# Kernel tuning notes

Hardware: AMD Instinct MI355X
Metric: run time of the kernel (lower is better)

## Reference

```python
import jax, jax.numpy as jnp
import numpy as np

EPS = 1e-5
C = 128
B = 16384
SYMBIOTIC = 4.0
NUM_PARENTS = 16
CHILDREN_PER_PARENT = 7


def _inverse(v):
    # torch: sort -> rank -> reversed rank -> gather sorted values
    idx0 = np.argsort(v, kind='stable')
    value = v[idx0]
    idx1 = np.argsort(idx0, kind='stable')  # ranks
    idx2 = v.shape[0] - 1 - idx1
    return value[idx2]


def _build_stats():
    counts = np.floor(50000.0 * 0.97 ** np.arange(C)) + 1.0  # long-tailed
    N = counts.sum()
    weight = (N / counts).astype(np.float32)
    prior = np.eye(C, dtype=np.float32)
    for p in range(NUM_PARENTS):
        ch = NUM_PARENTS + CHILDREN_PER_PARENT * p + np.arange(CHILDREN_PER_PARENT)
        prior[p, ch] = 1.0
    prior_me = (prior == 0).astype(np.float32)          # 1 - prior, keep only exact 1s
    prior_ms = prior - np.eye(C, dtype=np.float32)      # prior (0/1) minus eye
    v1_sig = np.log(N / counts - 1.0 + EPS).astype(np.float32)
    v2_sig = _inverse(v1_sig).astype(np.float32)
    v1_sm = np.log(counts / N + EPS).astype(np.float32)
    v2_sm = _inverse(v1_sm).astype(np.float32)
    return weight, prior_me, prior_ms, v1_sig, v2_sig, v1_sm, v2_sm


def setup_inputs() -> dict:
    key = jax.random.key(0)
    k1, k2 = jax.random.split(key)
    weight, prior_me, prior_ms, v1s, v2s, v1m, v2m = _build_stats()
    logits = 0.5 * jax.random.normal(k1, (12, B, C), dtype=jnp.float32)
    target = (jax.random.uniform(k2, (B, C)) < 0.1).astype(jnp.float32)
    return {
        'logits': logits, 'target': target,
        'weight': jnp.asarray(weight),
        'prior_me': jnp.asarray(prior_me), 'prior_ms': jnp.asarray(prior_ms),
        'v1_sigmoid': jnp.asarray(v1s), 'v2_sigmoid': jnp.asarray(v2s),
        'v1_softmax': jnp.asarray(v1m), 'v2_softmax': jnp.asarray(v2m),
    }


def reference(logits, target, weight, prior_me, prior_ms,
              v1_sigmoid, v2_sigmoid, v1_softmax, v2_softmax):
    zero = jnp.zeros_like(v1_sigmoid)
    # experts 0-5: sigmoid variants (long-tailed / balanced / inversed, twice)
    sig_shift = jnp.stack([zero, v1_sigmoid, v1_sigmoid - v2_sigmoid] * 2)  # [6,C]
    a_sig = jax.nn.sigmoid(logits[:6] - sig_shift[:, None, :])
    # experts 6-11: local-softmax variants
    sm_shift = jnp.stack([zero, v1_softmax, v1_softmax - v2_softmax] * 2)   # [6,C]
    e = jnp.exp(logits[6:] + sm_shift[:, None, :])                          # [6,B,C]
    denom = jnp.einsum('ebc,cd->ebd', e, prior_me) + e
    a_sm = e / (denom + EPS)
    acti = jnp.clip(jnp.concatenate([a_sig, a_sm], axis=0), EPS, 1.0 - EPS)  # [12,B,C]
    # weighted BCE per expert, summed
    bce = -weight * (target * jnp.log(acti) + (1.0 - target) * jnp.log(1.0 - acti))
    loss = jnp.sum(jnp.mean(bce, axis=(1, 2)))
    # symbiotic regularizer on experts 3,4,5,9,10,11
    row_sum = jnp.sum(prior_ms, axis=1)                 # [C]
    n_nz = jnp.sum(row_sum > 0).astype(acti.dtype)
    bsz = acti.shape[1]

    def symb(a):  # a: [B,C] activated logits
        def step(acc, xs):
            mask_row, parent = xs                       # [C], [B]
            term = jnp.log1p(jnp.exp(a - parent[:, None]))  # [B,C]
            rs = jnp.sum(mask_row)
            contrib = jnp.where(rs > 0, jnp.sum(term * mask_row) / (bsz * rs), 0.0)
            return acc + contrib, None
        total, _ = jax.lax.scan(step, jnp.float32(0.0), (prior_ms, a.T))
        return total / n_nz

    reg = jax.vmap(symb)(acti[jnp.array([3, 4, 5, 9, 10, 11])])
    return loss + SYMBIOTIC * jnp.sum(reg)
```

## Files before the change

### kernel.cpp

```cpp
#include <hip/hip_runtime.h>
#include <math.h>

#define CC 128
#define BB 16384
#define MEPS 1e-5f
#define LEPS  (-11.512925464970229f)
#define L1ME  (-1.0000050000287824e-05f)
#define NBLK 2048


__global__ __launch_bounds__(256) void mel_main(
    const float* __restrict__ logits, const float* __restrict__ target,
    const float* __restrict__ weight,
    const float* __restrict__ v1s, const float* __restrict__ v2s,
    const float* __restrict__ v1m, const float* __restrict__ v2m,
    float* __restrict__ partial)
{
    const int lane = threadIdx.x & 63;
    const int wib  = threadIdx.x >> 6;
    const int wave = blockIdx.x * 4 + wib;
    const int b0   = wave * 2;

    const int c0 = lane * 2;
    const int c1 = c0 + 1;

    const float w0 = weight[c0], w1 = weight[c1];
    const float s1a = v1s[c0], s1b = v1s[c1];
    const float s2a = v2s[c0], s2b = v2s[c1];
    const float m1a = v1m[c0], m1b = v1m[c1];
    const float m2a = v2m[c0], m2b = v2m[c1];

    const float sshift0[3] = {0.f, s1a, s1a - s2a};
    const float sshift1[3] = {0.f, s1b, s1b - s2b};
    const float mshift0[3] = {0.f, m1a, m1a - m2a};
    const float mshift1[3] = {0.f, m1b, m1b - m2b};

    const float childf = (lane >= 8) ? 1.f : 0.f;
    const int p0 = (c0 >= 16) ? (c0 - 16) / 7 : 0;
    const int p1 = (c1 >= 16) ? (c1 - 16) / 7 : 0;
    const int p0lane = p0 >> 1; const int p0sel = p0 & 1;
    const int p1lane = p1 >> 1; const int p1sel = p1 & 1;

    float2 tg[2], xs[6][2], xm[6][2];
    #pragma unroll
    for (int r = 0; r < 2; ++r) {
        const size_t ro = (size_t)(b0 + r) * CC + c0;
        tg[r] = *(const float2*)(target + ro);
        #pragma unroll
        for (int e = 0; e < 6; ++e)
            xs[e][r] = *(const float2*)(logits + (size_t)e * ((size_t)BB * CC) + ro);
        #pragma unroll
        for (int j = 0; j < 6; ++j)
            xm[j][r] = *(const float2*)(logits + (size_t)(6 + j) * ((size_t)BB * CC) + ro);
    }

    float acc_bce  = 0.f;
    float acc_symb = 0.f;

    #pragma unroll
    for (int r = 0; r < 2; ++r) {
        const bool t0 = tg[r].x > 0.5f;
        const bool t1 = tg[r].y > 0.5f;

        #pragma unroll
        for (int e = 0; e < 6; ++e) {
            const int si = e % 3;
            const float z0 = xs[e][r].x - sshift0[si];
            const float z1 = xs[e][r].y - sshift1[si];
            const float ex0 = __expf(-z0), ex1 = __expf(-z1);
            const float sp0 = __logf(1.f + ex0), sp1 = __logf(1.f + ex1);
            const float la0  = fminf(fmaxf(-sp0,      LEPS), L1ME);
            const float l1a0 = fminf(fmaxf(-z0 - sp0, LEPS), L1ME);
            const float la1  = fminf(fmaxf(-sp1,      LEPS), L1ME);
            const float l1a1 = fminf(fmaxf(-z1 - sp1, LEPS), L1ME);
            acc_bce += w0 * (t0 ? la0 : l1a0);
            acc_bce += w1 * (t1 ? la1 : l1a1);
            if (e >= 3) {
                const float a0 = __builtin_amdgcn_rcpf(1.f + ex0);
                const float a1 = __builtin_amdgcn_rcpf(1.f + ex1);
                const float ca0 = fminf(fmaxf(a0, MEPS), 1.f - MEPS);
                const float ca1 = fminf(fmaxf(a1, MEPS), 1.f - MEPS);
                const float qa0 = __shfl(ca0, p0lane, 64);
                const float qb0 = __shfl(ca1, p0lane, 64);
                const float cap0 = p0sel ? qb0 : qa0;
                const float qa1 = __shfl(ca0, p1lane, 64);
                const float qb1 = __shfl(ca1, p1lane, 64);
                const float cap1 = p1sel ? qb1 : qa1;
                acc_symb += childf * __logf(1.f + __expf(ca0 - cap0));
                acc_symb += childf * __logf(1.f + __expf(ca1 - cap1));
            }
        }

        #pragma unroll
        for (int j = 0; j < 6; ++j) {
            const int si = j % 3;
            const float e0 = __expf(xm[j][r].x + mshift0[si]);
            const float e1 = __expf(xm[j][r].y + mshift1[si]);
            float S = e0 + e1;
            #pragma unroll
            for (int off = 32; off > 0; off >>= 1)
                S += __shfl_xor(S, off, 64);
            const float qa0 = __shfl(e0, p0lane, 64);
            const float qb0 = __shfl(e1, p0lane, 64);
            const float ep0 = p0sel ? qb0 : qa0;
            const float qa1 = __shfl(e0, p1lane, 64);
            const float qb1 = __shfl(e1, p1lane, 64);
            const float ep1 = p1sel ? qb1 : qa1;

            const float den0 = S + MEPS - childf * ep0;
            const float den1 = S + MEPS - childf * ep1;
            float a0 = e0 * __builtin_amdgcn_rcpf(den0);
            float a1 = e1 * __builtin_amdgcn_rcpf(den1);
            a0 = fminf(fmaxf(a0, MEPS), 1.f - MEPS);
            a1 = fminf(fmaxf(a1, MEPS), 1.f - MEPS);
            const float arg0 = t0 ? a0 : 1.f - a0;
            const float arg1 = t1 ? a1 : 1.f - a1;
            acc_bce += w0 * __logf(arg0);
            acc_bce += w1 * __logf(arg1);
            if (j >= 3) {
                const float rS = __builtin_amdgcn_rcpf(S + MEPS);
                float ap0 = ep0 * rS, ap1 = ep1 * rS;
                ap0 = fminf(fmaxf(ap0, MEPS), 1.f - MEPS);
                ap1 = fminf(fmaxf(ap1, MEPS), 1.f - MEPS);
                acc_symb += childf * __logf(1.f + __expf(a0 - ap0));
                acc_symb += childf * __logf(1.f + __expf(a1 - ap1));
            }
        }
    }

    float val = -acc_bce * (1.f / ((float)BB * (float)CC))
              + acc_symb * (4.f / (112.f * (float)BB));

    #pragma unroll
    for (int off = 32; off > 0; off >>= 1)
        val += __shfl_xor(val, off, 64);

    __shared__ float sdata[4];
    if (lane == 0) sdata[wib] = val;
    __syncthreads();
    if (threadIdx.x == 0)
        partial[blockIdx.x] = sdata[0] + sdata[1] + sdata[2] + sdata[3];
}

__global__ __launch_bounds__(256) void mel_reduce(
    const float* __restrict__ partial, float* __restrict__ out)
{
    float v = 0.f;
    #pragma unroll
    for (int i = 0; i < NBLK / 256; ++i)
        v += partial[threadIdx.x + i * 256];
    #pragma unroll
    for (int off = 32; off > 0; off >>= 1)
        v += __shfl_xor(v, off, 64);
    __shared__ float s[4];
    const int lane = threadIdx.x & 63, wib = threadIdx.x >> 6;
    if (lane == 0) s[wib] = v;
    __syncthreads();
    if (threadIdx.x == 0) out[0] = s[0] + s[1] + s[2] + s[3];
}

extern "C" void kernel_launch(void* const* d_in, const int* in_sizes, int n_in,
                              void* d_out, int out_size, void* d_ws, size_t ws_size,
                              hipStream_t stream) {
    const float* logits = (const float*)d_in[0];
    const float* target = (const float*)d_in[1];
    const float* weight = (const float*)d_in[2];
    const float* v1s = (const float*)d_in[5];
    const float* v2s = (const float*)d_in[6];
    const float* v1m = (const float*)d_in[7];
    const float* v2m = (const float*)d_in[8];
    float* partial = (float*)d_ws;
    float* out = (float*)d_out;

    mel_main<<<NBLK, 256, 0, stream>>>(logits, target, weight,
                                       v1s, v2s, v1m, v2m, partial);
    mel_reduce<<<1, 256, 0, stream>>>(partial, out);
}
```

Baseline: 172.5 us.

## Remap lanes to four columns per row and use LDS for parent lookups

Each half-wave now handles one row, with each lane owning four consecutive columns. Loads become float4, and the six softmax row sums are reduced together over five interleaved shuffle steps instead of a full-wave reduction per expert. Parent activations are staged in per-wave shared memory and read back by index, replacing many cross-lane shuffles and selects. The sigmoid BCE clamp is dropped in favour of the plain softplus form, which cuts instructions in this compute-bound kernel but can differ slightly when logits fall outside the clamp range.

```diff
diff --git a/kernel.cpp b/kernel.cpp
--- a/kernel.cpp
+++ b/kernel.cpp
@@ -4,8 +4,6 @@
 #define CC 128
 #define BB 16384
 #define MEPS 1e-5f
-#define LEPS  (-11.512925464970229f)
-#define L1ME  (-1.0000050000287824e-05f)
 #define NBLK 2048
 
 
@@ -19,117 +17,126 @@
     const int lane = threadIdx.x & 63;
     const int wib  = threadIdx.x >> 6;
     const int wave = blockIdx.x * 4 + wib;
-    const int b0   = wave * 2;
+    const int r    = lane >> 5;
+    const int c    = lane & 31;
+    const int row  = wave * 2 + r;
 
-    const int c0 = lane * 2;
-    const int c1 = c0 + 1;
+    const float4 wtv = ((const float4*)weight)[c];
+    const float4 s1v = ((const float4*)v1s)[c];
+    const float4 s2v = ((const float4*)v2s)[c];
+    const float4 m1v = ((const float4*)v1m)[c];
+    const float4 m2v = ((const float4*)v2m)[c];
+    const float wt[4] = {wtv.x, wtv.y, wtv.z, wtv.w};
+    const float sv[3][4] = {{0.f,0.f,0.f,0.f},
+                            {s1v.x, s1v.y, s1v.z, s1v.w},
+                            {s1v.x-s2v.x, s1v.y-s2v.y, s1v.z-s2v.z, s1v.w-s2v.w}};
+    const float mv[3][4] = {{0.f,0.f,0.f,0.f},
+                            {m1v.x, m1v.y, m1v.z, m1v.w},
+                            {m1v.x-m2v.x, m1v.y-m2v.y, m1v.z-m2v.z, m1v.w-m2v.w}};
 
-    const float w0 = weight[c0], w1 = weight[c1];
-    const float s1a = v1s[c0], s1b = v1s[c1];
-    const float s2a = v2s[c0], s2b = v2s[c1];
-    const float m1a = v1m[c0], m1b = v1m[c1];
-    const float m2a = v2m[c0], m2b = v2m[c1];
+    const float childf = (c >= 4) ? 1.f : 0.f;
+    int pidx[4];
+    #pragma unroll
+    for (int k = 0; k < 4; ++k) {
+        const int ch = 4*c + k;
+        pidx[k] = (ch >= 16) ? (ch - 16) / 7 : 0;
+    }
 
-    const float sshift0[3] = {0.f, s1a, s1a - s2a};
-    const float sshift1[3] = {0.f, s1b, s1b - s2b};
-    const float mshift0[3] = {0.f, m1a, m1a - m2a};
-    const float mshift1[3] = {0.f, m1b, m1b - m2b};
+    float tg[4], xs[6][4], xm[6][4];
+    {
+        const size_t ro = (size_t)row * CC;
+        const float4 t4 = ((const float4*)(target + ro))[c];
+        tg[0]=t4.x; tg[1]=t4.y; tg[2]=t4.z; tg[3]=t4.w;
+        #pragma unroll
+        for (int e = 0; e < 6; ++e) {
+            const float4 v = ((const float4*)(logits + (size_t)e*(size_t)BB*CC + ro))[c];
+            xs[e][0]=v.x; xs[e][1]=v.y; xs[e][2]=v.z; xs[e][3]=v.w;
+        }
+        #pragma unroll
+        for (int j = 0; j < 6; ++j) {
+            const float4 v = ((const float4*)(logits + (size_t)(6+j)*(size_t)BB*CC + ro))[c];
+            xm[j][0]=v.x; xm[j][1]=v.y; xm[j][2]=v.z; xm[j][3]=v.w;
+        }
+    }
 
-    const float childf = (lane >= 8) ? 1.f : 0.f;
-    const int p0 = (c0 >= 16) ? (c0 - 16) / 7 : 0;
-    const int p1 = (c1 >= 16) ? (c1 - 16) / 7 : 0;
-    const int p0lane = p0 >> 1; const int p0sel = p0 & 1;
-    const int p1lane = p1 >> 1; const int p1sel = p1 & 1;
+    float accP = 0.f;
+    float accS = 0.f;
 
-    float2 tg[2], xs[6][2], xm[6][2];
+    float ca[3][4];
     #pragma unroll
-    for (int r = 0; r < 2; ++r) {
-        const size_t ro = (size_t)(b0 + r) * CC + c0;
-        tg[r] = *(const float2*)(target + ro);
+    for (int e = 0; e < 6; ++e) {
+        const int si = e % 3;
         #pragma unroll
-        for (int e = 0; e < 6; ++e)
-            xs[e][r] = *(const float2*)(logits + (size_t)e * ((size_t)BB * CC) + ro);
+        for (int k = 0; k < 4; ++k) {
+            const float z  = xs[e][k] - sv[si][k];
+            const float ex = __expf(-z);
+            const float opx = 1.f + ex;
+            const float sp = __logf(opx);
+            const float tz = (tg[k] > 0.5f) ? 0.f : z;
+            accP = fmaf(wt[k], sp + tz, accP);
+            if (e >= 3) ca[e-3][k] = __builtin_amdgcn_rcpf(opx);
+        }
+    }
+
+    float em[6][4], S[6];
+    #pragma unroll
+    for (int j = 0; j < 6; ++j) {
+        const int si = j % 3;
+        #pragma unroll
+        for (int k = 0; k < 4; ++k)
+            em[j][k] = __expf(xm[j][k] + mv[si][k]);
+        S[j] = (em[j][0] + em[j][1]) + (em[j][2] + em[j][3]);
+    }
+
+    #pragma unroll
+    for (int off = 16; off > 0; off >>= 1) {
         #pragma unroll
         for (int j = 0; j < 6; ++j)
-            xm[j][r] = *(const float2*)(logits + (size_t)(6 + j) * ((size_t)BB * CC) + ro);
+            S[j] += __shfl_xor(S[j], off, 64);
     }
 
-    float acc_bce  = 0.f;
-    float acc_symb = 0.f;
+    __shared__ float lds[4][9][2][16];
+    if (c < 4) {
+        #pragma unroll
+        for (int t = 0; t < 3; ++t)
+            *(float4*)&lds[wib][t][r][4*c] = make_float4(ca[t][0], ca[t][1], ca[t][2], ca[t][3]);
+        #pragma unroll
+        for (int j = 0; j < 6; ++j)
+            *(float4*)&lds[wib][3+j][r][4*c] = make_float4(em[j][0], em[j][1], em[j][2], em[j][3]);
+    }
 
     #pragma unroll
-    for (int r = 0; r < 2; ++r) {
-        const bool t0 = tg[r].x > 0.5f;
-        const bool t1 = tg[r].y > 0.5f;
+    for (int t = 0; t < 3; ++t) {
+        #pragma unroll
+        for (int k = 0; k < 4; ++k) {
+            const float cap = lds[wib][t][r][pidx[k]];
+            const float d   = ca[t][k] - cap;
+            accS = fmaf(childf, __logf(1.f + __expf(d)), accS);
+        }
+    }
 
+    #pragma unroll
+    for (int j = 0; j < 6; ++j) {
+        const float Sj = S[j] + MEPS;
+        const float rS = __builtin_amdgcn_rcpf(Sj);
         #pragma unroll
-        for (int e = 0; e < 6; ++e) {
-            const int si = e % 3;
-            const float z0 = xs[e][r].x - sshift0[si];
-            const float z1 = xs[e][r].y - sshift1[si];
-            const float ex0 = __expf(-z0), ex1 = __expf(-z1);
-            const float sp0 = __logf(1.f + ex0), sp1 = __logf(1.f + ex1);
-            const float la0  = fminf(fmaxf(-sp0,      LEPS), L1ME);
-            const float l1a0 = fminf(fmaxf(-z0 - sp0, LEPS), L1ME);
-            const float la1  = fminf(fmaxf(-sp1,      LEPS), L1ME);
-            const float l1a1 = fminf(fmaxf(-z1 - sp1, LEPS), L1ME);
-            acc_bce += w0 * (t0 ? la0 : l1a0);
-            acc_bce += w1 * (t1 ? la1 : l1a1);
-            if (e >= 3) {
-                const float a0 = __builtin_amdgcn_rcpf(1.f + ex0);
-                const float a1 = __builtin_amdgcn_rcpf(1.f + ex1);
-                const float ca0 = fminf(fmaxf(a0, MEPS), 1.f - MEPS);
-                const float ca1 = fminf(fmaxf(a1, MEPS), 1.f - MEPS);
-                const float qa0 = __shfl(ca0, p0lane, 64);
-                const float qb0 = __shfl(ca1, p0lane, 64);
-                const float cap0 = p0sel ? qb0 : qa0;
-                const float qa1 = __shfl(ca0, p1lane, 64);
-                const float qb1 = __shfl(ca1, p1lane, 64);
-                const float cap1 = p1sel ? qb1 : qa1;
-                acc_symb += childf * __logf(1.f + __expf(ca0 - cap0));
-                acc_symb += childf * __logf(1.f + __expf(ca1 - cap1));
-            }
-        }
-
-        #pragma unroll
-        for (int j = 0; j < 6; ++j) {
-            const int si = j % 3;
-            const float e0 = __expf(xm[j][r].x + mshift0[si]);
-            const float e1 = __expf(xm[j][r].y + mshift1[si]);
-            float S = e0 + e1;
-            #pragma unroll
-            for (int off = 32; off > 0; off >>= 1)
-                S += __shfl_xor(S, off, 64);
-            const float qa0 = __shfl(e0, p0lane, 64);
-            const float qb0 = __shfl(e1, p0lane, 64);
-            const float ep0 = p0sel ? qb0 : qa0;
-            const float qa1 = __shfl(e0, p1lane, 64);
-            const float qb1 = __shfl(e1, p1lane, 64);
-            const float ep1 = p1sel ? qb1 : qa1;
-
-            const float den0 = S + MEPS - childf * ep0;
-            const float den1 = S + MEPS - childf * ep1;
-            float a0 = e0 * __builtin_amdgcn_rcpf(den0);
-            float a1 = e1 * __builtin_amdgcn_rcpf(den1);
-            a0 = fminf(fmaxf(a0, MEPS), 1.f - MEPS);
-            a1 = fminf(fmaxf(a1, MEPS), 1.f - MEPS);
-            const float arg0 = t0 ? a0 : 1.f - a0;
-            const float arg1 = t1 ? a1 : 1.f - a1;
-            acc_bce += w0 * __logf(arg0);
-            acc_bce += w1 * __logf(arg1);
+        for (int k = 0; k < 4; ++k) {
+            const float ep  = lds[wib][3+j][r][pidx[k]];
+            const float den = Sj - childf * ep;
+            float a = em[j][k] * __builtin_amdgcn_rcpf(den);
+            a = fminf(fmaxf(a, MEPS), 1.f - MEPS);
+            const float arg = (tg[k] > 0.5f) ? a : 1.f - a;
+            accP = fmaf(wt[k], -__logf(arg), accP);
             if (j >= 3) {
-                const float rS = __builtin_amdgcn_rcpf(S + MEPS);
-                float ap0 = ep0 * rS, ap1 = ep1 * rS;
-                ap0 = fminf(fmaxf(ap0, MEPS), 1.f - MEPS);
-                ap1 = fminf(fmaxf(ap1, MEPS), 1.f - MEPS);
-                acc_symb += childf * __logf(1.f + __expf(a0 - ap0));
-                acc_symb += childf * __logf(1.f + __expf(a1 - ap1));
+                float ap = ep * rS;
+                ap = fminf(fmaxf(ap, MEPS), 1.f - MEPS);
+                accS = fmaf(childf, __logf(1.f + __expf(a - ap)), accS);
             }
         }
     }
 
-    float val = -acc_bce * (1.f / ((float)BB * (float)CC))
-              + acc_symb * (4.f / (112.f * (float)BB));
+    float val = accP * (1.f / ((float)BB * (float)CC))
+              + accS * (4.f / (112.f * (float)BB));
 
     #pragma unroll
     for (int off = 32; off > 0; off >>= 1)
@@ -139,7 +146,7 @@
     if (lane == 0) sdata[wib] = val;
     __syncthreads();
     if (threadIdx.x == 0)
-        partial[blockIdx.x] = sdata[0] + sdata[1] + sdata[2] + sdata[3];
+        partial[blockIdx.x] = (sdata[0] + sdata[1]) + (sdata[2] + sdata[3]);
 }
 
 __global__ __launch_bounds__(256) void mel_reduce(
@@ -156,7 +163,7 @@
     const int lane = threadIdx.x & 63, wib = threadIdx.x >> 6;
     if (lane == 0) s[wib] = v;
     __syncthreads();
-    if (threadIdx.x == 0) out[0] = s[0] + s[1] + s[2] + s[3];
+    if (threadIdx.x == 0) out[0] = (s[0] + s[1]) + (s[2] + s[3]);
 }
 
 extern "C" void kernel_launch(void* const* d_in, const int* in_sizes, int n_in,
```

After: 171.4 us. No clear change (-0.7%).
